# Optimization experiments

Hardware: AMD Instinct MI355X
Metric: run time of the kernel (lower is better)

The kernel has to match this reference:

```python
import jax, jax.numpy as jnp
import numpy as np
import math

B, D_MODEL, EMB, ORDER, SEQ = 4, 64, 33, 64, 256
TARGET, FAST_PCT, SLOW_PCT = 0.01, 0.3, 1.5


def _pos_emb(L, emb_dim):
    # PositionalEmbedding: t in [0,1], complex exponential bands
    t = jnp.linspace(0.0, 1.0, L)[None, :, None]                     # [1,L,1]
    bands = (emb_dim - 1) // 2
    t_r = jnp.linspace(0.0, L - 1.0, L)[None, :, None]
    w = 2.0 * math.pi * t_r / L
    f = jnp.linspace(1e-4, bands - 1.0, bands)[None, None]
    zc = jnp.exp(-1j * f * w)
    z = jnp.concatenate([t, zc.real, zc.imag], axis=-1)              # [1,L,emb_dim]
    return z.astype(jnp.float32), t.astype(jnp.float32)


def setup_inputs() -> dict:
    key = jax.random.key(0)
    ks = jax.random.split(key, 24)
    z, _ = _pos_emb(SEQ, EMB)

    def lin(k, fan_in, fan_out):
        return jax.random.normal(k, (fan_in, fan_out), jnp.float32) / np.sqrt(fan_in)

    inp = {
        'x': jax.random.normal(ks[0], (B, D_MODEL, SEQ, SEQ), jnp.float32),
        'z': z,
        'Xw1': lin(ks[1], EMB, ORDER), 'Xb1': jax.random.normal(ks[2], (ORDER,), jnp.float32) * 0.02,
        'Xw2': lin(ks[3], ORDER, ORDER), 'Xb2': jax.random.normal(ks[4], (ORDER,), jnp.float32) * 0.02,
        'Xw3': lin(ks[5], ORDER, ORDER), 'Xb3': jax.random.normal(ks[6], (ORDER,), jnp.float32) * 0.02,
        'Xwo': lin(ks[7], ORDER, D_MODEL),
        'Xfreq': jnp.ones((1, ORDER), jnp.float32),  # Sin freq, w=1, shared across layers
        'Yw1': lin(ks[8], EMB, ORDER), 'Yb1': jax.random.normal(ks[9], (ORDER,), jnp.float32) * 0.02,
        'Yw2': lin(ks[10], ORDER, ORDER), 'Yb2': jax.random.normal(ks[11], (ORDER,), jnp.float32) * 0.02,
        'Yw3': lin(ks[12], ORDER, ORDER), 'Yb3': jax.random.normal(ks[13], (ORDER,), jnp.float32) * 0.02,
        'Ywo': lin(ks[14], ORDER, D_MODEL),
        'Yfreq': jnp.ones((1, ORDER), jnp.float32),
        'bias': jax.random.normal(ks[15], (D_MODEL,), jnp.float32),
        'L': SEQ,
    }
    return inp


def _implicit_filter(z, w1, b1, w2, b2, w3, b3, wo, freq, t, deltas):
    # MLP with shared Sin activation, then exponential modulation (shift=0)
    h = jnp.sin(freq * (z @ w1 + b1))
    h = jnp.sin(freq * (h @ w2 + b2))
    h = jnp.sin(freq * (h @ w3 + b3))
    h = h @ wo                                   # [1,L,d_model]
    decay = jnp.exp(-t * jnp.abs(deltas))        # [1,L,d_model]
    return h * decay


def reference(x, z, Xw1, Xb1, Xw2, Xb2, Xw3, Xb3, Xwo, Xfreq,
              Yw1, Yb1, Yw2, Yb2, Yw3, Yb3, Ywo, Yfreq, bias, L):
    d_model = x.shape[1]
    t = jnp.linspace(0.0, 1.0, L)[None, :, None].astype(jnp.float32)
    max_dec = math.log(TARGET) / FAST_PCT
    min_dec = math.log(TARGET) / SLOW_PCT
    deltas = jnp.linspace(min_dec, max_dec, d_model)[None, None].astype(jnp.float32)

    hx = _implicit_filter(z, Xw1, Xb1, Xw2, Xb2, Xw3, Xb3, Xwo, Xfreq, t, deltas)
    hy = _implicit_filter(z, Yw1, Yb1, Yw2, Yb2, Yw3, Yb3, Ywo, Yfreq, t, deltas)
    # separable outer-product 2D kernel: [1,L,L,d_model] -> [d_model,L,L]
    k = jnp.einsum('ijk,imk->ijmk', hx, hy)[0]
    k = jnp.transpose(k, (2, 0, 1))

    fft_size = 2 * L
    k_f = jnp.fft.rfft2(k, s=(fft_size, fft_size)) / fft_size       # [D, 2L, L+1]
    u_f = jnp.fft.rfft2(x.astype(jnp.float32), s=(fft_size, fft_size))  # [B, D, 2L, L+1]
    y = jnp.fft.irfft2(u_f * k_f, s=(fft_size, fft_size))[..., :L, :L]
    out = y + x * bias[:, None, None]
    return out.astype(x.dtype)
```

## Files before the change

### kernel.cpp

```cpp
#include <hip/hip_runtime.h>

#define SL 256
#define RSTRIDE 312

typedef _Float16 f16;
typedef _Float16 f16x8 __attribute__((ext_vector_type(8)));
typedef _Float16 f16x4 __attribute__((ext_vector_type(4)));
typedef float f32x4 __attribute__((ext_vector_type(4)));

__global__ __launch_bounds__(64) void k_filters(
    const float* __restrict__ z,
    const float* __restrict__ Xw1, const float* __restrict__ Xb1,
    const float* __restrict__ Xw2, const float* __restrict__ Xb2,
    const float* __restrict__ Xw3, const float* __restrict__ Xb3,
    const float* __restrict__ Xwo, const float* __restrict__ Xfreq,
    const float* __restrict__ Yw1, const float* __restrict__ Yb1,
    const float* __restrict__ Yw2, const float* __restrict__ Yb2,
    const float* __restrict__ Yw3, const float* __restrict__ Yb3,
    const float* __restrict__ Ywo, const float* __restrict__ Yfreq,
    f16* __restrict__ hxT, f16* __restrict__ hyT)
{
    const int l = blockIdx.x;
    const int sel = blockIdx.y;
    const int t = threadIdx.x;
    const float* w1 = sel ? Yw1 : Xw1;  const float* b1 = sel ? Yb1 : Xb1;
    const float* w2 = sel ? Yw2 : Xw2;  const float* b2 = sel ? Yb2 : Xb2;
    const float* w3 = sel ? Yw3 : Xw3;  const float* b3 = sel ? Yb3 : Xb3;
    const float* wo = sel ? Ywo : Xwo;  const float* freq = sel ? Yfreq : Xfreq;
    f16* hT = sel ? hyT : hxT;

    __shared__ float zb[33];
    __shared__ float ha[64];
    __shared__ float hb[64];

    if (t < 33) zb[t] = z[l * 33 + t];
    __syncthreads();

    const float fr = freq[t];
    float s = b1[t];
    for (int k = 0; k < 33; ++k) s += zb[k] * w1[k * 64 + t];
    ha[t] = sinf(fr * s);
    __syncthreads();

    s = b2[t];
    for (int k = 0; k < 64; ++k) s += ha[k] * w2[k * 64 + t];
    hb[t] = sinf(fr * s);
    __syncthreads();

    s = b3[t];
    for (int k = 0; k < 64; ++k) s += hb[k] * w3[k * 64 + t];
    ha[t] = sinf(fr * s);
    __syncthreads();

    s = 0.f;
    for (int k = 0; k < 64; ++k) s += ha[k] * wo[k * 64 + t];

    const float MIN_DEC = -3.0701134573253937f;
    const float MAX_DEC = -15.350567286626968f;
    float ad = fabsf(MIN_DEC + (MAX_DEC - MIN_DEC) * ((float)t / 63.0f));
    float tl = (float)l / 255.0f;
    hT[t * 256 + l] = (f16)(s * expf(-tl * ad));
}

__device__ __forceinline__ f16x8 cvt8(float4 a, float4 b)
{
    f16x8 h;
    h[0] = (f16)a.x; h[1] = (f16)a.y; h[2] = (f16)a.z; h[3] = (f16)a.w;
    h[4] = (f16)b.x; h[5] = (f16)b.y; h[6] = (f16)b.z; h[7] = (f16)b.w;
    return h;
}

__device__ __forceinline__ void build_R(f16* R, const f16* __restrict__ hc,
                                        int tid)
{
    for (int idx = tid; idx < 8 * RSTRIDE; idx += 512) {
        int c = idx / RSTRIDE;
        int k = idx - c * RSTRIDE;
        int u = k + c;
        R[idx] = (u <= 255) ? hc[255 - u] : (f16)0.f;
    }
}

template<int J0>
__device__ __forceinline__ void phase1(
    const float* __restrict__ xr0, const float* __restrict__ xr1,
    const f16* __restrict__ R, f32x4 (&acc)[16], int ln, int quad)
{
    constexpr int QS = (J0 == 0) ? 4 : 8;
    float4 a0 = *(const float4*)xr0;
    float4 a1 = *(const float4*)(xr0 + 4);
    float4 b0 = *(const float4*)xr1;
    float4 b1 = *(const float4*)(xr1 + 4);

#pragma unroll
    for (int s = 0; s < QS; ++s) {
        const int q0 = s * 32;
        f16x8 af0 = cvt8(a0, a1);
        f16x8 af1 = cvt8(b0, b1);
        if (s + 1 < QS) {
            a0 = *(const float4*)(xr0 + q0 + 32);
            a1 = *(const float4*)(xr0 + q0 + 36);
            b0 = *(const float4*)(xr1 + q0 + 32);
            b1 = *(const float4*)(xr1 + q0 + 36);
        }
#pragma unroll
        for (int c8 = 0; c8 < 8; ++c8) {
            if (32 * s <= J0 + c8 * 16 + 15) {
                int j = J0 + c8 * 16 + ln;
                int s0 = 255 - j + q0 + quad * 8;
                int c = s0 & 7;
                f16x8 bf = *(const f16x8*)&R[c * RSTRIDE + (s0 - c)];
                acc[c8] = __builtin_amdgcn_mfma_f32_16x16x32_f16(
                    af0, bf, acc[c8], 0, 0, 0);
                acc[8 + c8] = __builtin_amdgcn_mfma_f32_16x16x32_f16(
                    af1, bf, acc[8 + c8], 0, 0, 0);
            }
        }
    }
}

__global__ __launch_bounds__(512, 4) void k_conv1(
    const float* __restrict__ x, const f16* __restrict__ hyT,
    f16* __restrict__ M)
{
    const int bd = blockIdx.x & 255;
    const int j0 = (blockIdx.x >> 8) << 7;
    const int d  = bd & 63;
    const int tid  = threadIdx.x;
    const int lane = tid & 63;
    const int wave = tid >> 6;
    const int ln   = lane & 15;
    const int quad = lane >> 4;

    __shared__ __align__(16) f16 Ry[8 * RSTRIDE];
    build_R(Ry, hyT + d * 256, tid);

    f32x4 acc[16];
#pragma unroll
    for (int a = 0; a < 16; ++a) acc[a] = (f32x4){0.f, 0.f, 0.f, 0.f};

    __syncthreads();

    const float* xr0 = x + (size_t)bd * (SL * SL) + (wave * 32 + ln) * SL + quad * 8;
    const float* xr1 = xr0 + 16 * SL;
    if (j0 == 0) phase1<0>(xr0, xr1, Ry, acc, ln, quad);
    else         phase1<128>(xr0, xr1, Ry, acc, ln, quad);

    f16* Mb = M + (size_t)bd * (SL * SL);
#pragma unroll
    for (int r = 0; r < 2; ++r)
#pragma unroll
        for (int c8 = 0; c8 < 8; ++c8) {
            int jl = j0 + c8 * 16 + ln;
            int pb = wave * 32 + r * 16 + quad * 4;
            f32x4 a = acc[r * 8 + c8];
            f16x4 v;
            v[0] = (f16)a[0]; v[1] = (f16)a[1];
            v[2] = (f16)a[2]; v[3] = (f16)a[3];
            *(f16x4*)&Mb[jl * 256 + pb] = v;
        }
}

__global__ __launch_bounds__(512, 4) void k_conv2(
    const float* __restrict__ x, const f16* __restrict__ M,
    const f16* __restrict__ hxT, const float* __restrict__ bias,
    float* __restrict__ out)
{
    const int bd = blockIdx.x & 255;
    const int jh = blockIdx.x >> 8;
    const int d  = bd & 63;
    const int tid  = threadIdx.x;
    const int lane = tid & 63;
    const int wave = tid >> 6;
    const int ln   = lane & 15;
    const int quad = lane >> 4;

    __shared__ __align__(16) f16 Rx[8 * RSTRIDE];
    build_R(Rx, hxT + d * 256, tid);

    f32x4 acc[16];
#pragma unroll
    for (int a = 0; a < 16; ++a) acc[a] = (f32x4){0.f, 0.f, 0.f, 0.f};

    __syncthreads();

    const int igrp = wave & 3;
    const int jgrp = wave >> 2;
    const f16* Mb = M + (size_t)bd * (SL * SL) + (size_t)(jh * 128 + jgrp * 64) * 256;
    const int nst = (igrp + 1) * 2;

    for (int s = 0; s < nst; ++s) {
        const int p0 = s * 32;
        f16x8 af[4];
#pragma unroll
        for (int rt = 0; rt < 4; ++rt)
            af[rt] = *(const f16x8*)&Mb[(rt * 16 + ln) * 256 + p0 + quad * 8];
#pragma unroll
        for (int ct = 0; ct < 4; ++ct) {
            if (p0 <= igrp * 64 + ct * 16 + 15) {
                int i = igrp * 64 + ct * 16 + ln;
                int s0 = 255 - i + p0 + quad * 8;
                int c = s0 & 7;
                f16x8 bf = *(const f16x8*)&Rx[c * RSTRIDE + (s0 - c)];
#pragma unroll
                for (int rt = 0; rt < 4; ++rt)
                    acc[rt * 4 + ct] = __builtin_amdgcn_mfma_f32_16x16x32_f16(
                        af[rt], bf, acc[rt * 4 + ct], 0, 0, 0);
            }
        }
    }

    const float bv = bias[d];
    const float sc = 1.0f / 512.0f;
    const float* xbd = x + (size_t)bd * (SL * SL);
    float* obd = out + (size_t)bd * (SL * SL);
#pragma unroll
    for (int rt = 0; rt < 4; ++rt)
#pragma unroll
        for (int ct = 0; ct < 4; ++ct) {
            int i = igrp * 64 + ct * 16 + ln;
            int j = jh * 128 + jgrp * 64 + rt * 16 + quad * 4;
            f32x4 a = acc[rt * 4 + ct];
            float4 xv = *(const float4*)(xbd + i * SL + j);
            float4 o;
            o.x = a[0] * sc + xv.x * bv;
            o.y = a[1] * sc + xv.y * bv;
            o.z = a[2] * sc + xv.z * bv;
            o.w = a[3] * sc + xv.w * bv;
            *(float4*)(obd + i * SL + j) = o;
        }
}

__global__ __launch_bounds__(512, 4) void k_fused(
    const float* __restrict__ x, const f16* __restrict__ hxT,
    const f16* __restrict__ hyT, const float* __restrict__ bias,
    float* __restrict__ out)
{
    const int bd = blockIdx.x & 255;
    const int j0 = (blockIdx.x >> 8) << 7;
    const int d  = bd & 63;
    const int tid  = threadIdx.x;
    const int lane = tid & 63;
    const int wave = tid >> 6;
    const int ln   = lane & 15;
    const int quad = lane >> 4;

    __shared__ __align__(16) f16 tmp[128 * 256];
    __shared__ __align__(16) f16 R[8 * RSTRIDE];

    const float* xbd = x + (size_t)bd * (SL * SL);

    build_R(R, hyT + d * 256, tid);

    f32x4 acc[16];
#pragma unroll
    for (int a = 0; a < 16; ++a) acc[a] = (f32x4){0.f, 0.f, 0.f, 0.f};

    __syncthreads();

    {
        const float* xr0 = xbd + (wave * 32 + ln) * SL + quad * 8;
        const float* xr1 = xr0 + 16 * SL;
        if (j0 == 0) phase1<0>(xr0, xr1, R, acc, ln, quad);
        else         phase1<128>(xr0, xr1, R, acc, ln, quad);

#pragma unroll
        for (int r = 0; r < 2; ++r)
#pragma unroll
            for (int c8 = 0; c8 < 8; ++c8) {
                int jl = c8 * 16 + ln;
                int pb = wave * 32 + r * 16 + quad * 4;
                f32x4 a = acc[r * 8 + c8];
                f16x4 v;
                v[0] = (f16)a[0]; v[1] = (f16)a[1];
                v[2] = (f16)a[2]; v[3] = (f16)a[3];
                *(f16x4*)&tmp[jl * 256 + (pb ^ ((jl & 7) << 3))] = v;
            }
    }

    __syncthreads();
    build_R(R, hxT + d * 256, tid);
#pragma unroll
    for (int a = 0; a < 16; ++a) acc[a] = (f32x4){0.f, 0.f, 0.f, 0.f};
    __syncthreads();

    const int igrp = wave & 3;
    const int jgrp = wave >> 2;
    const int nst = (igrp + 1) * 2;
    for (int s = 0; s < nst; ++s) {
        const int p0 = s * 32;
        f16x8 af[4];
#pragma unroll
        for (int rt = 0; rt < 4; ++rt) {
            int jl = jgrp * 64 + rt * 16 + ln;
            int off = (p0 + quad * 8) ^ ((jl & 7) << 3);
            af[rt] = *(const f16x8*)&tmp[jl * 256 + off];
        }
#pragma unroll
        for (int ct = 0; ct < 4; ++ct) {
            if (p0 <= igrp * 64 + ct * 16 + 15) {
                int i = igrp * 64 + ct * 16 + ln;
                int s0 = 255 - i + p0 + quad * 8;
                int c = s0 & 7;
                f16x8 bf = *(const f16x8*)&R[c * RSTRIDE + (s0 - c)];
#pragma unroll
                for (int rt = 0; rt < 4; ++rt)
                    acc[rt * 4 + ct] = __builtin_amdgcn_mfma_f32_16x16x32_f16(
                        af[rt], bf, acc[rt * 4 + ct], 0, 0, 0);
            }
        }
    }

    const float bv = bias[d];
    const float sc = 1.0f / 512.0f;
    float* obd = out + (size_t)bd * (SL * SL);
#pragma unroll
    for (int rt = 0; rt < 4; ++rt)
#pragma unroll
        for (int ct = 0; ct < 4; ++ct) {
            int i = igrp * 64 + ct * 16 + ln;
            int j = j0 + jgrp * 64 + rt * 16 + quad * 4;
            f32x4 a = acc[rt * 4 + ct];
            float4 xv = *(const float4*)(xbd + i * SL + j);
            float4 o;
            o.x = a[0] * sc + xv.x * bv;
            o.y = a[1] * sc + xv.y * bv;
            o.z = a[2] * sc + xv.z * bv;
            o.w = a[3] * sc + xv.w * bv;
            *(float4*)(obd + i * SL + j) = o;
        }
}

extern "C" void kernel_launch(void* const* d_in, const int* in_sizes, int n_in,
                              void* d_out, int out_size, void* d_ws, size_t ws_size,
                              hipStream_t stream)
{
    (void)in_sizes; (void)n_in; (void)out_size;
    const float* x     = (const float*)d_in[0];
    const float* z     = (const float*)d_in[1];
    const float* Xw1   = (const float*)d_in[2];
    const float* Xb1   = (const float*)d_in[3];
    const float* Xw2   = (const float*)d_in[4];
    const float* Xb2   = (const float*)d_in[5];
    const float* Xw3   = (const float*)d_in[6];
    const float* Xb3   = (const float*)d_in[7];
    const float* Xwo   = (const float*)d_in[8];
    const float* Xfreq = (const float*)d_in[9];
    const float* Yw1   = (const float*)d_in[10];
    const float* Yb1   = (const float*)d_in[11];
    const float* Yw2   = (const float*)d_in[12];
    const float* Yb2   = (const float*)d_in[13];
    const float* Yw3   = (const float*)d_in[14];
    const float* Yb3   = (const float*)d_in[15];
    const float* Ywo   = (const float*)d_in[16];
    const float* Yfreq = (const float*)d_in[17];
    const float* bias  = (const float*)d_in[18];

    f16* hxT = (f16*)d_ws;
    f16* hyT = hxT + 64 * 256;
    const size_t filt_bytes = 2u * 64 * 256 * sizeof(f16);
    const size_t M_bytes    = (size_t)256 * 256 * 256 * sizeof(f16);

    k_filters<<<dim3(256, 2), 64, 0, stream>>>(
        z, Xw1, Xb1, Xw2, Xb2, Xw3, Xb3, Xwo, Xfreq,
        Yw1, Yb1, Yw2, Yb2, Yw3, Yb3, Ywo, Yfreq, hxT, hyT);

    if (ws_size >= filt_bytes + M_bytes) {
        f16* M = (f16*)((char*)d_ws + filt_bytes);
        k_conv1<<<512, 512, 0, stream>>>(x, hyT, M);
        k_conv2<<<512, 512, 0, stream>>>(x, M, hxT, bias, (float*)d_out);
    } else {
        k_fused<<<512, 512, 0, stream>>>(x, hxT, hyT, bias, (float*)d_out);
    }
}
```

Before: 191.0 us.

## Fuse both separable convolution passes into one 1024-thread block per plane

Replaces the two-kernel path, which wrote a 32 MB f16 intermediate to global memory between passes, with a single kernel that gives each (batch, channel) plane its own 1024-thread block. The whole 256x256 f16 intermediate is held in LDS (about 138 KB of dynamic shared memory). This removes the global round trip and the duplicated x reads. In exchange only 256 blocks run, one per CU at most, which lowers occupancy and parallelism. The kernel also depends on the large dynamic LDS allocation succeeding and falls back to the old fused kernel if it does not.

```diff
diff --git a/kernel.cpp b/kernel.cpp
--- a/kernel.cpp
+++ b/kernel.cpp
@@ -70,15 +70,135 @@
     return h;
 }
 
+template<int NT>
 __device__ __forceinline__ void build_R(f16* R, const f16* __restrict__ hc,
                                         int tid)
 {
-    for (int idx = tid; idx < 8 * RSTRIDE; idx += 512) {
+    for (int idx = tid; idx < 8 * RSTRIDE; idx += NT) {
         int c = idx / RSTRIDE;
         int k = idx - c * RSTRIDE;
         int u = k + c;
         R[idx] = (u <= 255) ? hc[255 - u] : (f16)0.f;
     }
+}
+
+__global__ __launch_bounds__(1024, 4) void k_one(
+    const float* __restrict__ x, const f16* __restrict__ hxT,
+    const f16* __restrict__ hyT, const float* __restrict__ bias,
+    float* __restrict__ out)
+{
+    extern __shared__ __align__(16) f16 smem[];
+    f16* tmp = smem;
+    f16* Ry  = smem + 256 * 256;
+    f16* Rx  = Ry + 8 * RSTRIDE;
+
+    const int bd = blockIdx.x;
+    const int d  = bd & 63;
+    const int tid  = threadIdx.x;
+    const int lane = tid & 63;
+    const int wave = tid >> 6;
+    const int ln   = lane & 15;
+    const int quad = lane >> 4;
+
+    const float* xbd = x + (size_t)bd * (SL * SL);
+
+    build_R<1024>(Ry, hyT + d * 256, tid);
+
+    f32x4 acc[16];
+#pragma unroll
+    for (int a = 0; a < 16; ++a) acc[a] = (f32x4){0.f, 0.f, 0.f, 0.f};
+
+    __syncthreads();
+
+    {
+        const float* xr = xbd + (wave * 16 + ln) * SL + quad * 8;
+        float4 a0 = *(const float4*)xr;
+        float4 a1 = *(const float4*)(xr + 4);
+
+#pragma unroll
+        for (int s = 0; s < 8; ++s) {
+            const int q0 = s * 32;
+            f16x8 af = cvt8(a0, a1);
+            if (s + 1 < 8) {
+                a0 = *(const float4*)(xr + q0 + 32);
+                a1 = *(const float4*)(xr + q0 + 36);
+            }
+#pragma unroll
+            for (int c8 = 0; c8 < 16; ++c8) {
+                if (32 * s <= c8 * 16 + 15) {
+                    int j = c8 * 16 + ln;
+                    int s0 = 255 - j + q0 + quad * 8;
+                    int c = s0 & 7;
+                    f16x8 bf = *(const f16x8*)&Ry[c * RSTRIDE + (s0 - c)];
+                    acc[c8] = __builtin_amdgcn_mfma_f32_16x16x32_f16(
+                        af, bf, acc[c8], 0, 0, 0);
+                }
+            }
+        }
+
+#pragma unroll
+        for (int c8 = 0; c8 < 16; ++c8) {
+            int jl = c8 * 16 + ln;
+            int pb = wave * 16 + quad * 4;
+            f32x4 a = acc[c8];
+            f16x4 v;
+            v[0] = (f16)a[0]; v[1] = (f16)a[1];
+            v[2] = (f16)a[2]; v[3] = (f16)a[3];
+            *(f16x4*)&tmp[jl * 256 + (pb ^ ((jl & 7) << 3))] = v;
+        }
+    }
+
+    build_R<1024>(Rx, hxT + d * 256, tid);
+#pragma unroll
+    for (int a = 0; a < 16; ++a) acc[a] = (f32x4){0.f, 0.f, 0.f, 0.f};
+
+    __syncthreads();
+
+    const int igrp = wave & 3;
+    const int jgrp = wave >> 2;
+    const int nst = (igrp + 1) * 2;
+    for (int s = 0; s < nst; ++s) {
+        const int p0 = s * 32;
+        f16x8 af[4];
+#pragma unroll
+        for (int rt = 0; rt < 4; ++rt) {
+            int jl = jgrp * 64 + rt * 16 + ln;
+            int off = (p0 + quad * 8) ^ ((jl & 7) << 3);
+            af[rt] = *(const f16x8*)&tmp[jl * 256 + off];
+        }
+#pragma unroll
+        for (int ct = 0; ct < 4; ++ct) {
+            if (p0 <= igrp * 64 + ct * 16 + 15) {
+                int i = igrp * 64 + ct * 16 + ln;
+                int s0 = 255 - i + p0 + quad * 8;
+                int c = s0 & 7;
+                f16x8 bf = *(const f16x8*)&Rx[c * RSTRIDE + (s0 - c)];
+#pragma unroll
+                for (int rt = 0; rt < 4; ++rt)
+                    acc[rt * 4 + ct] = __builtin_amdgcn_mfma_f32_16x16x32_f16(
+                        af[rt], bf, acc[rt * 4 + ct], 0, 0, 0);
+            }
+        }
+    }
+
+    const float bv = bias[d];
+    const float sc = 1.0f / 512.0f;
+    float* obd = out + (size_t)bd * (SL * SL);
+#pragma unroll
+    for (int rt = 0; rt < 4; ++rt)
+#pragma unroll
+        for (int ct = 0; ct < 4; ++ct) {
+            int i = igrp * 64 + ct * 16 + ln;
+            int j = jgrp * 64 + rt * 16 + quad * 4;
+            f32x4 a = acc[rt * 4 + ct];
+            float4 xv = *(const float4*)(xbd + i * SL + j);
+            float4 o;
+            o.x = a[0] * sc + xv.x * bv;
+            o.y = a[1] * sc + xv.y * bv;
+            o.z = a[2] * sc + xv.z * bv;
+            o.w = a[3] * sc + xv.w * bv;
+            *(float4*)(obd + i * SL + j) = o;
+        }
 }
 
 template<int J0>
@@ -119,9 +239,10 @@
     }
 }
 
-__global__ __launch_bounds__(512, 4) void k_conv1(
-    const float* __restrict__ x, const f16* __restrict__ hyT,
-    f16* __restrict__ M)
+__global__ __launch_bounds__(512, 4) void k_fused(
+    const float* __restrict__ x, const f16* __restrict__ hxT,
+    const f16* __restrict__ hyT, const float* __restrict__ bias,
+    float* __restrict__ out)
 {
     const int bd = blockIdx.x & 255;
     const int j0 = (blockIdx.x >> 8) << 7;
@@ -132,125 +253,12 @@
     const int ln   = lane & 15;
     const int quad = lane >> 4;
 
-    __shared__ __align__(16) f16 Ry[8 * RSTRIDE];
-    build_R(Ry, hyT + d * 256, tid);
-
-    f32x4 acc[16];
-#pragma unroll
-    for (int a = 0; a < 16; ++a) acc[a] = (f32x4){0.f, 0.f, 0.f, 0.f};
-
-    __syncthreads();
-
-    const float* xr0 = x + (size_t)bd * (SL * SL) + (wave * 32 + ln) * SL + quad * 8;
-    const float* xr1 = xr0 + 16 * SL;
-    if (j0 == 0) phase1<0>(xr0, xr1, Ry, acc, ln, quad);
-    else         phase1<128>(xr0, xr1, Ry, acc, ln, quad);
-
-    f16* Mb = M + (size_t)bd * (SL * SL);
-#pragma unroll
-    for (int r = 0; r < 2; ++r)
-#pragma unroll
-        for (int c8 = 0; c8 < 8; ++c8) {
-            int jl = j0 + c8 * 16 + ln;
-            int pb = wave * 32 + r * 16 + quad * 4;
-            f32x4 a = acc[r * 8 + c8];
-            f16x4 v;
-            v[0] = (f16)a[0]; v[1] = (f16)a[1];
-            v[2] = (f16)a[2]; v[3] = (f16)a[3];
-            *(f16x4*)&Mb[jl * 256 + pb] = v;
-        }
-}
-
-__global__ __launch_bounds__(512, 4) void k_conv2(
-    const float* __restrict__ x, const f16* __restrict__ M,
-    const f16* __restrict__ hxT, const float* __restrict__ bias,
-    float* __restrict__ out)
-{
-    const int bd = blockIdx.x & 255;
-    const int jh = blockIdx.x >> 8;
-    const int d  = bd & 63;
-    const int tid  = threadIdx.x;
-    const int lane = tid & 63;
-    const int wave = tid >> 6;
-    const int ln   = lane & 15;
-    const int quad = lane >> 4;
-
-    __shared__ __align__(16) f16 Rx[8 * RSTRIDE];
-    build_R(Rx, hxT + d * 256, tid);
-
-    f32x4 acc[16];
-#pragma unroll
-    for (int a = 0; a < 16; ++a) acc[a] = (f32x4){0.f, 0.f, 0.f, 0.f};
-
-    __syncthreads();
-
-    const int igrp = wave & 3;
-    const int jgrp = wave >> 2;
-    const f16* Mb = M + (size_t)bd * (SL * SL) + (size_t)(jh * 128 + jgrp * 64) * 256;
-    const int nst = (igrp + 1) * 2;
-
-    for (int s = 0; s < nst; ++s) {
-        const int p0 = s * 32;
-        f16x8 af[4];
-#pragma unroll
-        for (int rt = 0; rt < 4; ++rt)
-            af[rt] = *(const f16x8*)&Mb[(rt * 16 + ln) * 256 + p0 + quad * 8];
-#pragma unroll
-        for (int ct = 0; ct < 4; ++ct) {
-            if (p0 <= igrp * 64 + ct * 16 + 15) {
-                int i = igrp * 64 + ct * 16 + ln;
-                int s0 = 255 - i + p0 + quad * 8;
-                int c = s0 & 7;
-                f16x8 bf = *(const f16x8*)&Rx[c * RSTRIDE + (s0 - c)];
-#pragma unroll
-                for (int rt = 0; rt < 4; ++rt)
-                    acc[rt * 4 + ct] = __builtin_amdgcn_mfma_f32_16x16x32_f16(
-                        af[rt], bf, acc[rt * 4 + ct], 0, 0, 0);
-            }
-        }
-    }
-
-    const float bv = bias[d];
-    const float sc = 1.0f / 512.0f;
-    const float* xbd = x + (size_t)bd * (SL * SL);
-    float* obd = out + (size_t)bd * (SL * SL);
-#pragma unroll
-    for (int rt = 0; rt < 4; ++rt)
-#pragma unroll
-        for (int ct = 0; ct < 4; ++ct) {
-            int i = igrp * 64 + ct * 16 + ln;
-            int j = jh * 128 + jgrp * 64 + rt * 16 + quad * 4;
-            f32x4 a = acc[rt * 4 + ct];
-            float4 xv = *(const float4*)(xbd + i * SL + j);
-            float4 o;
-            o.x = a[0] * sc + xv.x * bv;
-            o.y = a[1] * sc + xv.y * bv;
-            o.z = a[2] * sc + xv.z * bv;
-            o.w = a[3] * sc + xv.w * bv;
-            *(float4*)(obd + i * SL + j) = o;
-        }
-}
-
-__global__ __launch_bounds__(512, 4) void k_fused(
-    const float* __restrict__ x, const f16* __restrict__ hxT,
-    const f16* __restrict__ hyT, const float* __restrict__ bias,
-    float* __restrict__ out)
-{
-    const int bd = blockIdx.x & 255;
-    const int j0 = (blockIdx.x >> 8) << 7;
-    const int d  = bd & 63;
-    const int tid  = threadIdx.x;
-    const int lane = tid & 63;
-    const int wave = tid >> 6;
-    const int ln   = lane & 15;
-    const int quad = lane >> 4;
-
     __shared__ __align__(16) f16 tmp[128 * 256];
     __shared__ __align__(16) f16 R[8 * RSTRIDE];
 
     const float* xbd = x + (size_t)bd * (SL * SL);
 
-    build_R(R, hyT + d * 256, tid);
+    build_R<512>(R, hyT + d * 256, tid);
 
     f32x4 acc[16];
 #pragma unroll
@@ -279,7 +287,7 @@
     }
 
     __syncthreads();
-    build_R(R, hxT + d * 256, tid);
+    build_R<512>(R, hxT + d * 256, tid);
 #pragma unroll
     for (int a = 0; a < 16; ++a) acc[a] = (f32x4){0.f, 0.f, 0.f, 0.f};
     __syncthreads();
@@ -335,7 +343,7 @@
                               void* d_out, int out_size, void* d_ws, size_t ws_size,
                               hipStream_t stream)
 {
-    (void)in_sizes; (void)n_in; (void)out_size;
+    (void)in_sizes; (void)n_in; (void)out_size; (void)ws_size;
     const float* x     = (const float*)d_in[0];
     const float* z     = (const float*)d_in[1];
     const float* Xw1   = (const float*)d_in[2];
@@ -358,17 +366,17 @@
 
     f16* hxT = (f16*)d_ws;
     f16* hyT = hxT + 64 * 256;
-    const size_t filt_bytes = 2u * 64 * 256 * sizeof(f16);
-    const size_t M_bytes    = (size_t)256 * 256 * 256 * sizeof(f16);
 
     k_filters<<<dim3(256, 2), 64, 0, stream>>>(
         z, Xw1, Xb1, Xw2, Xb2, Xw3, Xb3, Xwo, Xfreq,
         Yw1, Yb1, Yw2, Yb2, Yw3, Yb3, Ywo, Yfreq, hxT, hyT);
 
-    if (ws_size >= filt_bytes + M_bytes) {
-        f16* M = (f16*)((char*)d_ws + filt_bytes);
-        k_conv1<<<512, 512, 0, stream>>>(x, hyT, M);
-        k_conv2<<<512, 512, 0, stream>>>(x, M, hxT, bias, (float*)d_out);
+    const int dyn_lds = (256 * 256 + 2 * 8 * RSTRIDE) * (int)sizeof(f16);
+    static hipError_t attr_rc = hipFuncSetAttribute(
+        (const void*)k_one, hipFuncAttributeMaxDynamicSharedMemorySize, dyn_lds);
+
+    if (attr_rc == hipSuccess) {
+        k_one<<<256, 1024, dyn_lds, stream>>>(x, hxT, hyT, bias, (float*)d_out);
     } else {
         k_fused<<<512, 512, 0, stream>>>(x, hxT, hyT, bias, (float*)d_out);
     }
```

After: 166.8 us. -12.7%, faster.
